# Optimization experiments

Measured on AMD Instinct MI355X. Metric: run time of the kernel, lower is better.

## Reference

```python
import jax, jax.numpy as jnp
import numpy as np

HIDDEN = 256
MAX_LENGTH = 256
NUM_LAYERS = 4
VOCAB = 50257


def setup_inputs() -> dict:
    key = jax.random.key(0)
    ks = jax.random.split(key, 16)
    s = 0.05
    return {
        "token": jax.random.randint(ks[0], (1,), 0, VOCAB, dtype=jnp.int64 if jax.config.jax_enable_x64 else jnp.int32),
        "hidden": jax.random.normal(ks[1], (NUM_LAYERS, 1, HIDDEN), dtype=jnp.float32),
        "encoder_outputs": jax.random.normal(ks[2], (MAX_LENGTH, HIDDEN), dtype=jnp.float32),
        "emb": jax.random.normal(ks[3], (VOCAB, HIDDEN), dtype=jnp.float32) * s,
        "attn_w": jax.random.normal(ks[4], (MAX_LENGTH, 2 * HIDDEN), dtype=jnp.float32) * s,
        "attn_b": jax.random.normal(ks[5], (MAX_LENGTH,), dtype=jnp.float32) * s,
        "comb_w": jax.random.normal(ks[6], (HIDDEN, 2 * HIDDEN), dtype=jnp.float32) * s,
        "comb_b": jax.random.normal(ks[7], (HIDDEN,), dtype=jnp.float32) * s,
        "gru_wih": jax.random.normal(ks[8], (NUM_LAYERS, 3 * HIDDEN, HIDDEN), dtype=jnp.float32) * s,
        "gru_whh": jax.random.normal(ks[9], (NUM_LAYERS, 3 * HIDDEN, HIDDEN), dtype=jnp.float32) * s,
        "gru_bih": jax.random.normal(ks[10], (NUM_LAYERS, 3 * HIDDEN), dtype=jnp.float32) * s,
        "gru_bhh": jax.random.normal(ks[11], (NUM_LAYERS, 3 * HIDDEN), dtype=jnp.float32) * s,
        "out_w": jax.random.normal(ks[12], (VOCAB, HIDDEN), dtype=jnp.float32) * s,
        "out_b": jax.random.normal(ks[13], (VOCAB,), dtype=jnp.float32) * s,
    }


def _gru_cell(x, h, wih, whh, bih, bhh):
    # PyTorch GRU cell: gates ordered [r, z, n]
    gi = x @ wih.T + bih  # [1, 3H]
    gh = h @ whh.T + bhh  # [1, 3H]
    i_r, i_z, i_n = jnp.split(gi, 3, axis=1)
    h_r, h_z, h_n = jnp.split(gh, 3, axis=1)
    r = jax.nn.sigmoid(i_r + h_r)
    z = jax.nn.sigmoid(i_z + h_z)
    n = jnp.tanh(i_n + r * h_n)
    return (1.0 - z) * n + z * h


def reference(token, hidden, encoder_outputs, emb, attn_w, attn_b, comb_w, comb_b,
              gru_wih, gru_whh, gru_bih, gru_bhh, out_w, out_b):
    # embedding lookup (dropout is identity in eval)  -> [1, H]
    embedded = emb[token]
    # Bahdanau-style attention weights over MAX_LENGTH positions
    attn_in = jnp.concatenate([embedded, hidden[0]], axis=1)  # [1, 2H]
    attn_weights = jax.nn.softmax(attn_in @ attn_w.T + attn_b, axis=1)  # [1, L]
    attn_applied = attn_weights @ encoder_outputs  # [1, H]
    comb_in = jnp.concatenate([embedded, attn_applied], axis=1)  # [1, 2H]
    x = jax.nn.relu(comb_in @ comb_w.T + comb_b)  # [1, H]
    # 4-layer GRU, single timestep
    new_h = []
    for l in range(NUM_LAYERS):
        h_l = _gru_cell(x, hidden[l], gru_wih[l], gru_whh[l], gru_bih[l], gru_bhh[l])
        new_h.append(h_l)
        x = h_l
    hidden_new = jnp.stack(new_h, axis=0)  # [4, 1, H]
    logp = jax.nn.log_softmax(x @ out_w.T + out_b, axis=1)  # [1, V]
    return (logp, hidden_new, attn_weights)
```

## Files before the change

kernel.cpp:

```cpp
#include <hip/hip_runtime.h>
#include <hip/hip_bf16.h>

#define H 256
#define L2H 512
#define NLAYERS 4
#define VOCAB 50257

#define OUT_LOGP 0
#define OUT_HID  50257
#define OUT_ATTN 51281

#define WS_SCORE  0
#define WS_BARS   256
#define WS_APP    512
#define WS_X0     768
#define WS_X1     1024
#define WS_PM     1280
#define WS_PS     1792
#define WS_FLAG   2304

#define NBLK 256

#define C_SCORE 0
#define C_APP   1
#define C_X(l)  (2 + (l))
#define C_LOG   7

typedef unsigned short u16;

__device__ __forceinline__ float bf2f(u16 u) {
    return __uint_as_float(((unsigned int)u) << 16);
}

__device__ __forceinline__ u16 f2bf(float f) {
    unsigned int x = __float_as_uint(f);
    unsigned int r = x + 0x7fff + ((x >> 16) & 1);
    return (u16)(r >> 16);
}

template<bool BF16>
__device__ __forceinline__ float ld1(const void* p, size_t i) {
    if (BF16) return bf2f(((const u16*)p)[i]);
    else      return ((const float*)p)[i];
}

template<bool BF16>
__device__ __forceinline__ float4 ld4(const void* p, size_t i) {
    if (BF16) {
        ushort4 w = *(const ushort4*)((const u16*)p + i);
        return make_float4(bf2f(w.x), bf2f(w.y), bf2f(w.z), bf2f(w.w));
    } else {
        return *(const float4*)((const float*)p + i);
    }
}

template<bool BF16>
__device__ __forceinline__ void ld8(const void* p, size_t i, float* f) {
    if (BF16) {
        uint4 u = *(const uint4*)((const u16*)p + i);
        f[0] = bf2f(u.x & 0xffff); f[1] = bf2f(u.x >> 16);
        f[2] = bf2f(u.y & 0xffff); f[3] = bf2f(u.y >> 16);
        f[4] = bf2f(u.z & 0xffff); f[5] = bf2f(u.z >> 16);
        f[6] = bf2f(u.w & 0xffff); f[7] = bf2f(u.w >> 16);
    } else {
        const float4* q = (const float4*)((const float*)p + i);
        float4 a = q[0], b = q[1];
        f[0] = a.x; f[1] = a.y; f[2] = a.z; f[3] = a.w;
        f[4] = b.x; f[5] = b.y; f[6] = b.z; f[7] = b.w;
    }
}

template<bool BF16>
__device__ __forceinline__ void st(void* p, size_t i, float v) {
    if (BF16) ((u16*)p)[i] = f2bf(v);
    else      ((float*)p)[i] = v;
}

__device__ __forceinline__ float ldc(const float* p) {
    return __hip_atomic_load(const_cast<float*>(p), __ATOMIC_RELAXED, __HIP_MEMORY_SCOPE_AGENT);
}
__device__ __forceinline__ void stc(float* p, float v) {
    __hip_atomic_store(p, v, __ATOMIC_RELAXED, __HIP_MEMORY_SCOPE_AGENT);
}

__device__ __forceinline__ void arrive(unsigned* bars, int i) {
    __syncthreads();
    if (threadIdx.x == 0)
        __hip_atomic_fetch_add(&bars[i * 16], 1u, __ATOMIC_RELAXED, __HIP_MEMORY_SCOPE_AGENT);
}
__device__ __forceinline__ void wait_for(unsigned* bars, int i, unsigned exp) {
    if (threadIdx.x == 0) {
        while (__hip_atomic_load(&bars[i * 16], __ATOMIC_RELAXED, __HIP_MEMORY_SCOPE_AGENT) < exp)
            __builtin_amdgcn_s_sleep(2);
    }
    __syncthreads();
}

__global__ __launch_bounds__(256) void k_init(const void* emb, float* ws) {
    int tid = threadIdx.x;
    ((unsigned*)(ws + WS_BARS))[tid] = 0u;
    ws[WS_APP + tid] = 0.f;
    if (tid < 64) {
        float b = fabsf(bf2f(((const u16*)emb)[tid]));
        #pragma unroll
        for (int off = 32; off; off >>= 1) b = fmaxf(b, __shfl_xor(b, off));
        if (tid == 0) ws[WS_FLAG] = (b < 1.0f) ? 1.0f : 0.0f;
    }
}

template<bool BF16>
__device__ __forceinline__ void pipeline(
    const int* __restrict__ tok, const void* __restrict__ emb,
    const void* __restrict__ hidden,
    const void* __restrict__ attn_w, const void* __restrict__ attn_b,
    const void* __restrict__ enc,
    const void* __restrict__ comb_w, const void* __restrict__ comb_b,
    const void* __restrict__ gwih, const void* __restrict__ gwhh,
    const void* __restrict__ gbih, const void* __restrict__ gbhh,
    const void* __restrict__ out_w, const void* __restrict__ out_b,
    float* __restrict__ ws, void* __restrict__ out)
{
    unsigned* bars = (unsigned*)(ws + WS_BARS);
    const int tid  = threadIdx.x;
    const int lane = tid & 63;
    const int wid  = tid >> 6;
    const int bx   = blockIdx.x;
    const size_t es = BF16 ? 2 : 4;

    __shared__ float lds[256];
    __shared__ float wsm[256];

    if (bx < 64) {
        const int wv = (bx << 2) | wid;
        const int j8 = lane * 8;

        {
            float xin[8];
            if (lane < 32) ld8<BF16>(emb, (size_t)tok[0] * H + j8, xin);
            else           ld8<BF16>(hidden, (size_t)(j8 - H), xin);
            float wf[8]; ld8<BF16>(attn_w, (size_t)wv * L2H + j8, wf);
            float v = 0.f;
            #pragma unroll
            for (int q = 0; q < 8; ++q) v += xin[q] * wf[q];
            #pragma unroll
            for (int off = 32; off; off >>= 1) v += __shfl_xor(v, off);
            if (lane == 0) stc(ws + WS_SCORE + wv, v + ld1<BF16>(attn_b, wv));
        }
        arrive(bars, C_SCORE);

        if (bx < 16) {
            const int l0 = bx * 16;
            float ev[16];
            #pragma unroll
            for (int k = 0; k < 16; ++k)
                ev[k] = ld1<BF16>(enc, (size_t)(l0 + k) * H + tid);
            wait_for(bars, C_SCORE, 64);
            float s = ldc(ws + WS_SCORE + tid);
            lds[tid] = s; __syncthreads();
            for (int off = 128; off; off >>= 1) {
                if (tid < off) lds[tid] = fmaxf(lds[tid], lds[tid + off]);
                __syncthreads();
            }
            float M = lds[0]; __syncthreads();
            float e = __expf(s - M);
            lds[tid] = e; __syncthreads();
            for (int off = 128; off; off >>= 1) {
                if (tid < off) lds[tid] += lds[tid + off];
                __syncthreads();
            }
            float w = e / lds[0];
            wsm[tid] = w; __syncthreads();
            if (bx == 0) st<BF16>(out, OUT_ATTN + tid, w);
            float acc = 0.f;
            #pragma unroll
            for (int k = 0; k < 16; ++k) acc += wsm[l0 + k] * ev[k];
            atomicAdd(&ws[WS_APP + tid], acc);
            arrive(bars, C_APP);
        }

        {
            float wf[8]; ld8<BF16>(comb_w, (size_t)wv * L2H + j8, wf);
            float xin[8];
            if (lane < 32) ld8<BF16>(emb, (size_t)tok[0] * H + j8, xin);
            wait_for(bars, C_APP, 16);
            if (lane >= 32) {
                #pragma unroll
                for (int q = 0; q < 8; ++q) xin[q] = ldc(ws + WS_APP + (j8 - H) + q);
            }
            float v = 0.f;
            #pragma unroll
            for (int q = 0; q < 8; ++q) v += xin[q] * wf[q];
            #pragma unroll
            for (int off = 32; off; off >>= 1) v += __shfl_xor(v, off);
            if (lane == 0) stc(ws + WS_X0 + wv, fmaxf(v + ld1<BF16>(comb_b, wv), 0.f));
        }
        arrive(bars, C_X(0));

        const int e4 = lane * 4;
        #pragma unroll 1
        for (int l = 0; l < NLAYERS; ++l) {
            const float* xin_p = ws + ((l & 1) ? WS_X1 : WS_X0);
            float*       xout  = ws + ((l & 1) ? WS_X0 : WS_X1);
            const char* wih = (const char*)gwih + (size_t)l * 3 * H * H * es;
            const char* whh = (const char*)gwhh + (size_t)l * 3 * H * H * es;
            const char* bih = (const char*)gbih + (size_t)l * 3 * H * es;
            const char* bhh = (const char*)gbhh + (size_t)l * 3 * H * es;
            const char* hprev = (const char*)hidden + (size_t)l * H * es;
            char*       hout  = (char*)out + (size_t)(OUT_HID + l * H) * es;
            const int i = wv;

            float4 hv  = ld4<BF16>(hprev, e4);
            float4 wri = ld4<BF16>(wih, (size_t)(i        ) * H + e4);
            float4 wzi = ld4<BF16>(wih, (size_t)(H + i    ) * H + e4);
            float4 wni = ld4<BF16>(wih, (size_t)(2 * H + i) * H + e4);
            float4 wrh = ld4<BF16>(whh, (size_t)(i        ) * H + e4);
            float4 wzh = ld4<BF16>(whh, (size_t)(H + i    ) * H + e4);
            float4 wnh = ld4<BF16>(whh, (size_t)(2 * H + i) * H + e4);

            wait_for(bars, C_X(l), 64);

            float4 xv;
            xv.x = ldc(xin_p + e4);     xv.y = ldc(xin_p + e4 + 1);
            xv.z = ldc(xin_p + e4 + 2); xv.w = ldc(xin_p + e4 + 3);

            float a = wri.x * xv.x + wri.y * xv.y + wri.z * xv.z + wri.w * xv.w
                    + wrh.x * hv.x + wrh.y * hv.y + wrh.z * hv.z + wrh.w * hv.w;
            float b = wzi.x * xv.x + wzi.y * xv.y + wzi.z * xv.z + wzi.w * xv.w
                    + wzh.x * hv.x + wzh.y * hv.y + wzh.z * hv.z + wzh.w * hv.w;
            float c = wni.x * xv.x + wni.y * xv.y + wni.z * xv.z + wni.w * xv.w;
            float d = wnh.x * hv.x + wnh.y * hv.y + wnh.z * hv.z + wnh.w * hv.w;

            #pragma unroll
            for (int off = 32; off; off >>= 1) {
                a += __shfl_xor(a, off);
                b += __shfl_xor(b, off);
                c += __shfl_xor(c, off);
                d += __shfl_xor(d, off);
            }
            if (lane == 0) {
                float r = 1.f / (1.f + __expf(-(a + ld1<BF16>(bih, i) + ld1<BF16>(bhh, i))));
                float z = 1.f / (1.f + __expf(-(b + ld1<BF16>(bih, H + i) + ld1<BF16>(bhh, H + i))));
                float n = tanhf(c + ld1<BF16>(bih, 2 * H + i) + r * (d + ld1<BF16>(bhh, 2 * H + i)));
                float hold = ld1<BF16>(hprev, i);
                float hn = (1.f - z) * n + z * hold;
                stc(xout + i, hn);
                st<BF16>(hout, i, hn);
            }
            arrive(bars, C_X(l + 1));
        }
    }

    wait_for(bars, C_X(4), 64);

    const int grp = (bx << 3) | (tid >> 5);
    const int l32 = tid & 31;
    float vs[25];
    {
        float xf[8];
        #pragma unroll
        for (int q = 0; q < 8; ++q) xf[q] = ldc(ws + WS_X0 + l32 * 8 + q);

        float m = -1e30f, s = 0.f;
        #pragma unroll
        for (int it = 0; it < 3; ++it) {
            const int rb = it * 16384 + grp;
            float wf[8][8], bb[8];
            #pragma unroll
            for (int k = 0; k < 8; ++k) {
                ld8<BF16>(out_w, (size_t)(rb + (k << 11)) * H + l32 * 8, wf[k]);
                bb[k] = ld1<BF16>(out_b, rb + (k << 11));
            }
            #pragma unroll
            for (int k = 0; k < 8; ++k) {
                float v = wf[k][0]*xf[0] + wf[k][1]*xf[1] + wf[k][2]*xf[2] + wf[k][3]*xf[3]
                        + wf[k][4]*xf[4] + wf[k][5]*xf[5] + wf[k][6]*xf[6] + wf[k][7]*xf[7];
                #pragma unroll
                for (int off = 16; off; off >>= 1) v += __shfl_xor(v, off);
                v += bb[k];
                vs[it * 8 + k] = v;
                float mn = fmaxf(m, v);
                s = s * __expf(m - mn) + __expf(v - mn);
                m = mn;
            }
        }
        vs[24] = 0.f;
        if (grp < VOCAB - 49152) {
            int r = 49152 + grp;
            float wf[8]; ld8<BF16>(out_w, (size_t)r * H + l32 * 8, wf);
            float v = wf[0]*xf[0] + wf[1]*xf[1] + wf[2]*xf[2] + wf[3]*xf[3]
                    + wf[4]*xf[4] + wf[5]*xf[5] + wf[6]*xf[6] + wf[7]*xf[7];
            #pragma unroll
            for (int off = 16; off; off >>= 1) v += __shfl_xor(v, off);
            v += ld1<BF16>(out_b, r);
            vs[24] = v;
            float mn = fmaxf(m, v);
            s = s * __expf(m - mn) + __expf(v - mn);
            m = mn;
        }

        {
            float mo = __shfl_xor(m, 32), so = __shfl_xor(s, 32);
            float M = fmaxf(m, mo);
            s = s * __expf(m - M) + so * __expf(mo - M);
            m = M;
        }
        if (lane == 0) { lds[wid] = m; lds[4 + wid] = s; }
        __syncthreads();
        if (tid == 0) {
            float M01 = fmaxf(lds[0], lds[1]);
            float S01 = lds[4] * __expf(lds[0] - M01) + lds[5] * __expf(lds[1] - M01);
            float M23 = fmaxf(lds[2], lds[3]);
            float S23 = lds[6] * __expf(lds[2] - M23) + lds[7] * __expf(lds[3] - M23);
            float Mx = fmaxf(M01, M23);
            float S  = S01 * __expf(M01 - Mx) + S23 * __expf(M23 - Mx);
            stc(ws + WS_PM + bx, Mx);
            stc(ws + WS_PS + bx, S);
        }
    }
    arrive(bars, C_LOG);
    wait_for(bars, C_LOG, 256);

    {
        float m = ldc(ws + WS_PM + tid);
        float s = ldc(ws + WS_PS + tid);
        #pragma unroll
        for (int off = 32; off; off >>= 1) {
            float mo = __shfl_xor(m, off), so = __shfl_xor(s, off);
            float M = fmaxf(m, mo);
            s = s * __expf(m - M) + so * __expf(mo - M);
            m = M;
        }
        if (lane == 0) { lds[wid] = m; lds[4 + wid] = s; }
        __syncthreads();
        if (tid == 0) {
            float M01 = fmaxf(lds[0], lds[1]);
            float S01 = lds[4] * __expf(lds[0] - M01) + lds[5] * __expf(lds[1] - M01);
            float M23 = fmaxf(lds[2], lds[3]);
            float S23 = lds[6] * __expf(lds[2] - M23) + lds[7] * __expf(lds[3] - M23);
            float Mx = fmaxf(M01, M23);
            float S  = S01 * __expf(M01 - Mx) + S23 * __expf(M23 - Mx);
            lds[8] = Mx + __logf(S);
        }
        __syncthreads();
        float c = lds[8];
        if (l32 == 0) {
            #pragma unroll
            for (int it = 0; it < 3; ++it) {
                #pragma unroll
                for (int k = 0; k < 8; ++k)
                    st<BF16>(out, OUT_LOGP + it * 16384 + (k << 11) + grp, vs[it * 8 + k] - c);
            }
            if (grp < VOCAB - 49152)
                st<BF16>(out, OUT_LOGP + 49152 + grp, vs[24] - c);
        }
    }
}

__global__ __launch_bounds__(256, 1) void k_all(
    const int* __restrict__ tok, const void* __restrict__ emb,
    const void* __restrict__ hidden,
    const void* __restrict__ attn_w, const void* __restrict__ attn_b,
    const void* __restrict__ enc,
    const void* __restrict__ comb_w, const void* __restrict__ comb_b,
    const void* __restrict__ gwih, const void* __restrict__ gwhh,
    const void* __restrict__ gbih, const void* __restrict__ gbhh,
    const void* __restrict__ out_w, const void* __restrict__ out_b,
    float* __restrict__ ws, void* __restrict__ out)
{
    if (ws[WS_FLAG] > 0.5f)
        pipeline<true >(tok, emb, hidden, attn_w, attn_b, enc, comb_w, comb_b,
                        gwih, gwhh, gbih, gbhh, out_w, out_b, ws, out);
    else
        pipeline<false>(tok, emb, hidden, attn_w, attn_b, enc, comb_w, comb_b,
                        gwih, gwhh, gbih, gbhh, out_w, out_b, ws, out);
}

extern "C" void kernel_launch(void* const* d_in, const int* in_sizes, int n_in,
                              void* d_out, int out_size, void* d_ws, size_t ws_size,
                              hipStream_t stream) {
    const int* tok = (const int*)d_in[0];
    float* ws = (float*)d_ws;

    k_init<<<dim3(1), dim3(256), 0, stream>>>(d_in[3], ws);
    k_all<<<dim3(NBLK), dim3(256), 0, stream>>>(
        tok, d_in[3], d_in[1], d_in[4], d_in[5], d_in[2], d_in[6], d_in[7],
        d_in[8], d_in[9], d_in[10], d_in[11], d_in[12], d_in[13],
        ws, d_out);
}
```

Measured before the change: 174.0 us.

## Replace counter barriers with sentinel-flag dataflow sync and sharded final barrier

Every score and GRU-layer output slot is pre-filled with a NaN sentinel. Consumers now poll each value directly until it is written, instead of waiting on per-stage arrival counters, so the per-layer barriers (score, X0..X3) go away. Each layer gets its own buffer so the sentinels stay valid, and the softmax partial buffers now reuse freed regions. The final log-softmax barrier is split across 8 cache-line counters to reduce atomic contention. This costs more polling loads per lane and relies on NaN sentinel values never appearing as real outputs.

```diff
diff --git a/kernel.cpp b/kernel.cpp
--- a/kernel.cpp
+++ b/kernel.cpp
@@ -13,18 +13,17 @@
 #define WS_SCORE  0
 #define WS_BARS   256
 #define WS_APP    512
-#define WS_X0     768
-#define WS_X1     1024
-#define WS_PM     1280
-#define WS_PS     1792
+#define WS_X      768
+#define WS_PM     768
+#define WS_PS     1024
 #define WS_FLAG   2304
 
+#define CL_APP  0
+#define CL_X4   16
+#define CL_LOG  32
+
 #define NBLK 256
-
-#define C_SCORE 0
-#define C_APP   1
-#define C_X(l)  (2 + (l))
-#define C_LOG   7
+#define SENT 0x7FC00001u
 
 typedef unsigned short u16;
 
@@ -83,23 +82,42 @@
     __hip_atomic_store(p, v, __ATOMIC_RELAXED, __HIP_MEMORY_SCOPE_AGENT);
 }
 
-__device__ __forceinline__ void arrive(unsigned* bars, int i) {
+template<int SLP>
+__device__ __forceinline__ float pollf(const float* p) {
+    unsigned u = __hip_atomic_load((unsigned*)const_cast<float*>(p),
+                                   __ATOMIC_RELAXED, __HIP_MEMORY_SCOPE_AGENT);
+    while (u == SENT) {
+        __builtin_amdgcn_s_sleep(SLP);
+        u = __hip_atomic_load((unsigned*)const_cast<float*>(p),
+                              __ATOMIC_RELAXED, __HIP_MEMORY_SCOPE_AGENT);
+    }
+    return __uint_as_float(u);
+}
+
+__device__ __forceinline__ void arrive_line(unsigned* bars, int idx) {
     __syncthreads();
     if (threadIdx.x == 0)
-        __hip_atomic_fetch_add(&bars[i * 16], 1u, __ATOMIC_RELAXED, __HIP_MEMORY_SCOPE_AGENT);
-}
-__device__ __forceinline__ void wait_for(unsigned* bars, int i, unsigned exp) {
+        __hip_atomic_fetch_add(&bars[idx], 1u, __ATOMIC_RELAXED, __HIP_MEMORY_SCOPE_AGENT);
+}
+template<int SLP>
+__device__ __forceinline__ void wait_line(unsigned* bars, int idx, unsigned exp) {
     if (threadIdx.x == 0) {
-        while (__hip_atomic_load(&bars[i * 16], __ATOMIC_RELAXED, __HIP_MEMORY_SCOPE_AGENT) < exp)
-            __builtin_amdgcn_s_sleep(2);
+        while (__hip_atomic_load(&bars[idx], __ATOMIC_RELAXED, __HIP_MEMORY_SCOPE_AGENT) < exp)
+            __builtin_amdgcn_s_sleep(SLP);
     }
     __syncthreads();
 }
 
 __global__ __launch_bounds__(256) void k_init(const void* emb, float* ws) {
     int tid = threadIdx.x;
-    ((unsigned*)(ws + WS_BARS))[tid] = 0u;
-    ws[WS_APP + tid] = 0.f;
+    unsigned* bars = (unsigned*)(ws + WS_BARS);
+    __hip_atomic_store(&bars[tid], 0u, __ATOMIC_RELAXED, __HIP_MEMORY_SCOPE_AGENT);
+    __hip_atomic_store((unsigned*)(ws + WS_APP) + tid, 0u, __ATOMIC_RELAXED, __HIP_MEMORY_SCOPE_AGENT);
+    __hip_atomic_store((unsigned*)(ws + WS_SCORE) + tid, SENT, __ATOMIC_RELAXED, __HIP_MEMORY_SCOPE_AGENT);
+    #pragma unroll
+    for (int k = 0; k < 4; ++k)
+        __hip_atomic_store((unsigned*)(ws + WS_X + k * 256) + tid, SENT,
+                           __ATOMIC_RELAXED, __HIP_MEMORY_SCOPE_AGENT);
     if (tid < 64) {
         float b = fabsf(bf2f(((const u16*)emb)[tid]));
         #pragma unroll
@@ -135,10 +153,10 @@
         const int j8 = lane * 8;
 
         {
+            float wf[8]; ld8<BF16>(attn_w, (size_t)wv * L2H + j8, wf);
             float xin[8];
             if (lane < 32) ld8<BF16>(emb, (size_t)tok[0] * H + j8, xin);
             else           ld8<BF16>(hidden, (size_t)(j8 - H), xin);
-            float wf[8]; ld8<BF16>(attn_w, (size_t)wv * L2H + j8, wf);
             float v = 0.f;
             #pragma unroll
             for (int q = 0; q < 8; ++q) v += xin[q] * wf[q];
@@ -146,7 +164,6 @@
             for (int off = 32; off; off >>= 1) v += __shfl_xor(v, off);
             if (lane == 0) stc(ws + WS_SCORE + wv, v + ld1<BF16>(attn_b, wv));
         }
-        arrive(bars, C_SCORE);
 
         if (bx < 16) {
             const int l0 = bx * 16;
@@ -154,8 +171,7 @@
             #pragma unroll
             for (int k = 0; k < 16; ++k)
                 ev[k] = ld1<BF16>(enc, (size_t)(l0 + k) * H + tid);
-            wait_for(bars, C_SCORE, 64);
-            float s = ldc(ws + WS_SCORE + tid);
+            float s = pollf<1>(ws + WS_SCORE + tid);
             lds[tid] = s; __syncthreads();
             for (int off = 128; off; off >>= 1) {
                 if (tid < off) lds[tid] = fmaxf(lds[tid], lds[tid + off]);
@@ -175,14 +191,14 @@
             #pragma unroll
             for (int k = 0; k < 16; ++k) acc += wsm[l0 + k] * ev[k];
             atomicAdd(&ws[WS_APP + tid], acc);
-            arrive(bars, C_APP);
+            arrive_line(bars, CL_APP);
         }
 
         {
             float wf[8]; ld8<BF16>(comb_w, (size_t)wv * L2H + j8, wf);
             float xin[8];
             if (lane < 32) ld8<BF16>(emb, (size_t)tok[0] * H + j8, xin);
-            wait_for(bars, C_APP, 16);
+            wait_line<1>(bars, CL_APP, 16);
             if (lane >= 32) {
                 #pragma unroll
                 for (int q = 0; q < 8; ++q) xin[q] = ldc(ws + WS_APP + (j8 - H) + q);
@@ -192,15 +208,14 @@
             for (int q = 0; q < 8; ++q) v += xin[q] * wf[q];
             #pragma unroll
             for (int off = 32; off; off >>= 1) v += __shfl_xor(v, off);
-            if (lane == 0) stc(ws + WS_X0 + wv, fmaxf(v + ld1<BF16>(comb_b, wv), 0.f));
-        }
-        arrive(bars, C_X(0));
+            if (lane == 0) stc(ws + WS_X + wv, fmaxf(v + ld1<BF16>(comb_b, wv), 0.f));
+        }
 
         const int e4 = lane * 4;
         #pragma unroll 1
         for (int l = 0; l < NLAYERS; ++l) {
-            const float* xin_p = ws + ((l & 1) ? WS_X1 : WS_X0);
-            float*       xout  = ws + ((l & 1) ? WS_X0 : WS_X1);
+            const float* xin_p = ws + WS_X + l * 256;
+            float*       xout  = ws + WS_X + (l + 1) * 256;
             const char* wih = (const char*)gwih + (size_t)l * 3 * H * H * es;
             const char* whh = (const char*)gwhh + (size_t)l * 3 * H * H * es;
             const char* bih = (const char*)gbih + (size_t)l * 3 * H * es;
@@ -217,11 +232,11 @@
             float4 wzh = ld4<BF16>(whh, (size_t)(H + i    ) * H + e4);
             float4 wnh = ld4<BF16>(whh, (size_t)(2 * H + i) * H + e4);
 
-            wait_for(bars, C_X(l), 64);
-
             float4 xv;
-            xv.x = ldc(xin_p + e4);     xv.y = ldc(xin_p + e4 + 1);
-            xv.z = ldc(xin_p + e4 + 2); xv.w = ldc(xin_p + e4 + 3);
+            xv.x = pollf<2>(xin_p + e4);
+            xv.y = pollf<2>(xin_p + e4 + 1);
+            xv.z = pollf<2>(xin_p + e4 + 2);
+            xv.w = pollf<2>(xin_p + e4 + 3);
 
             float a = wri.x * xv.x + wri.y * xv.y + wri.z * xv.z + wri.w * xv.w
                     + wrh.x * hv.x + wrh.y * hv.y + wrh.z * hv.z + wrh.w * hv.w;
@@ -246,11 +261,11 @@
                 stc(xout + i, hn);
                 st<BF16>(hout, i, hn);
             }
-            arrive(bars, C_X(l + 1));
-        }
-    }
-
-    wait_for(bars, C_X(4), 64);
+        }
+        arrive_line(bars, CL_X4);
+    }
+
+    wait_line<2>(bars, CL_X4, 64);
 
     const int grp = (bx << 3) | (tid >> 5);
     const int l32 = tid & 31;
@@ -258,7 +273,7 @@
     {
         float xf[8];
         #pragma unroll
-        for (int q = 0; q < 8; ++q) xf[q] = ldc(ws + WS_X0 + l32 * 8 + q);
+        for (int q = 0; q < 8; ++q) xf[q] = ldc(ws + WS_X + 4 * 256 + l32 * 8 + q);
 
         float m = -1e30f, s = 0.f;
         #pragma unroll
@@ -317,8 +332,13 @@
             stc(ws + WS_PS + bx, S);
         }
     }
-    arrive(bars, C_LOG);
-    wait_for(bars, C_LOG, 256);
+    arrive_line(bars, CL_LOG + 16 * (bx & 7));
+    if (tid < 8) {
+        while (__hip_atomic_load(&bars[CL_LOG + 16 * tid],
+                                 __ATOMIC_RELAXED, __HIP_MEMORY_SCOPE_AGENT) < 32u)
+            __builtin_amdgcn_s_sleep(1);
+    }
+    __syncthreads();
 
     {
         float m = ldc(ws + WS_PM + tid);
```

New measurement: 173.7 us. Within noise of the previous version (-0.1%).
